# Performance work log

Measured on AMD Instinct MI355X. Metric: run time of the kernel, lower is better.

Reference implementation:

```python
import jax, jax.numpy as jnp
import numpy as np

WINDOW = 13

def setup_inputs() -> dict:
    key = jax.random.key(0)
    ks = jax.random.split(key, 5)
    B, C, D, H, W = 8, 64, 13, 64, 64
    c8 = C // 8
    x = jax.random.normal(ks[0], (B, C, D, H, W), dtype=jnp.float32)
    wq = jax.random.normal(ks[1], (c8, C), dtype=jnp.float32) * 0.1
    wk = jax.random.normal(ks[2], (c8, C), dtype=jnp.float32) * 0.1
    wv = jax.random.normal(ks[3], (C, C), dtype=jnp.float32) * 0.1
    bq = jnp.zeros((c8,), jnp.float32)
    bk = jnp.zeros((c8,), jnp.float32)
    bv = jnp.zeros((C,), jnp.float32)
    return {"x": x, "wq": wq, "bq": bq, "wk": wk, "bk": bk, "wv": wv, "bv": bv}

def reference(x, wq, bq, wk, bk, wv, bv):
    B, C, D, H, W = x.shape
    N = D * H * W
    nb = N // WINDOW  # N chosen divisible by WINDOW
    xf = x.reshape(B, C, N)
    # 1x1 Conv3d == per-voxel channel matmul
    q = jnp.einsum('oc,bcn->bon', wq, xf) + bq[None, :, None]
    k = jnp.einsum('oc,bcn->bon', wk, xf) + bk[None, :, None]
    v = jnp.einsum('oc,bcn->bon', wv, xf) + bv[None, :, None]
    # split flattened spatial dim into independent windows of size 13
    qb = q.reshape(B, -1, nb, WINDOW)
    kb = k.reshape(B, -1, nb, WINDOW)
    vb = v.reshape(B, C, nb, WINDOW)
    # scores[b,n,i,j] = sum_c q[b,c,n,i] * k[b,c,n,j]  (no scaling, as in source)
    scores = jnp.einsum('bcni,bcnj->bnij', qb, kb)
    att = jax.nn.softmax(scores, axis=-1)
    # out[b,c,n,i] = sum_j v[b,c,n,j] * att[b,n,i,j]  (v @ att^T per window)
    out = jnp.einsum('bcnj,bnij->bcni', vb, att)
    return out.reshape(B, C, D, H, W)
```

## Files before the change

### kernel.cpp

```cpp
#include <hip/hip_runtime.h>

#define WINDOW 13
#define NTOT   53248
#define WPB    8
#define VT     104
#define VS     112
#define WS     72
#define QKS    112
#define VPS    132

typedef float floatx4 __attribute__((ext_vector_type(4)));
typedef short shortx8 __attribute__((ext_vector_type(8)));

__device__ __forceinline__ unsigned short f2bf(float f) {
    union { float f; unsigned int u; } v; v.f = f;
    unsigned int u = v.u;
    unsigned int r = (u + 0x7fffu + ((u >> 16) & 1u)) >> 16;
    return (unsigned short)r;
}

__device__ __forceinline__ unsigned int pk2(float a, float b) {
    return (unsigned int)f2bf(a) | ((unsigned int)f2bf(b) << 16);
}

__global__ __launch_bounds__(512, 6)
void attn_win13_kernel(const float* __restrict__ x,
                       const float* __restrict__ wq, const float* __restrict__ bq,
                       const float* __restrict__ wk, const float* __restrict__ bk,
                       const float* __restrict__ wv, const float* __restrict__ bv,
                       float* __restrict__ out)
{
    __shared__ __align__(16) unsigned short xT[VS * WS];
    __shared__ __align__(16) unsigned short wbf[80 * WS];
    __shared__ float ball[80];
    __shared__ __align__(16) unsigned short vpad[64 * VPS];
    __shared__ __align__(16) float qk[16 * QKS];
    float* const att = (float*)wbf;
    unsigned short* const attb = (unsigned short*)qk;

    const int tid = threadIdx.x;
    const int b   = blockIdx.y;
    const int v0  = blockIdx.x * VT;
    const size_t total = (size_t)512 * NTOT;

    if (tid < 224) {
        const int vq = tid >> 3, cg8 = tid & 7;
        const int c0 = cg8 * 8, vx = vq * 4;
        float xv[4][8];
#pragma unroll
        for (int i = 0; i < 8; ++i) {
            size_t idx = (size_t)(b * 64 + c0 + i) * NTOT + v0 + vx;
            if (idx > total - 4) idx = total - 4;
            const float4 t = *(const float4*)(x + idx);
            xv[0][i] = t.x; xv[1][i] = t.y; xv[2][i] = t.z; xv[3][i] = t.w;
        }
#pragma unroll
        for (int r = 0; r < 4; ++r) {
            uint4 pk;
            pk.x = pk2(xv[r][0], xv[r][1]);
            pk.y = pk2(xv[r][2], xv[r][3]);
            pk.z = pk2(xv[r][4], xv[r][5]);
            pk.w = pk2(xv[r][6], xv[r][7]);
            *(uint4*)(&xT[(vx + r) * WS + c0]) = pk;
        }
    } else if (tid >= 256) {
        const int wf0 = tid - 256;
#pragma unroll
        for (int it = 0; it < 3; ++it) {
            const int wf = wf0 + (it << 8);
            if (wf < 640) {
                const int r = wf >> 3, cw = (wf & 7) * 8;
                const float* src = (r < 8)  ? (wq + r * 64 + cw)
                                 : (r < 16) ? (wk + (r - 8) * 64 + cw)
                                            : (wv + (r - 16) * 64 + cw);
                const float4 w0 = *(const float4*)src;
                const float4 w1 = *(const float4*)(src + 4);
                uint4 pk;
                pk.x = pk2(w0.x, w0.y); pk.y = pk2(w0.z, w0.w);
                pk.z = pk2(w1.x, w1.y); pk.w = pk2(w1.z, w1.w);
                *(uint4*)(&wbf[r * WS + cw]) = pk;
            }
        }
    }
    if (tid >= 432) {
        const int t2 = tid - 432;
        ball[t2] = (t2 < 8) ? bq[t2] : (t2 < 16) ? bk[t2 - 8] : bv[t2 - 16];
    }
    {
        const int r = tid >> 3, w = tid & 7;
        vpad[r * VPS + w * 16 + 13] = 0;
        *(unsigned int*)(&vpad[r * VPS + w * 16 + 14]) = 0u;
    }
    __syncthreads();

    {
        const int wid  = tid >> 6;
        const int lane = tid & 63;
        const int col  = lane & 15;
        const int g    = lane >> 4;
        for (int t = wid; t < 35; t += 8) {
            const int mt = t / 7, nt = t % 7;
            const shortx8 wa0 = *(const shortx8*)(&wbf[(mt * 16 + col) * WS + g * 8]);
            const shortx8 xa0 = *(const shortx8*)(&xT [(nt * 16 + col) * WS + g * 8]);
            const shortx8 wa1 = *(const shortx8*)(&wbf[(mt * 16 + col) * WS + 32 + g * 8]);
            const shortx8 xa1 = *(const shortx8*)(&xT [(nt * 16 + col) * WS + 32 + g * 8]);
            floatx4 acc = {0.f, 0.f, 0.f, 0.f};
            if (mt == 0) {
                acc = __builtin_amdgcn_mfma_f32_16x16x32_bf16(wa0, xa0, acc, 0, 0, 0);
                acc = __builtin_amdgcn_mfma_f32_16x16x32_bf16(wa1, xa1, acc, 0, 0, 0);
                const int row0 = g * 4;
                const int vox  = nt * 16 + col;
                qk[(row0 + 0) * QKS + vox] = acc[0] + ball[row0 + 0];
                qk[(row0 + 1) * QKS + vox] = acc[1] + ball[row0 + 1];
                qk[(row0 + 2) * QKS + vox] = acc[2] + ball[row0 + 2];
                qk[(row0 + 3) * QKS + vox] = acc[3] + ball[row0 + 3];
            } else {
                acc = __builtin_amdgcn_mfma_f32_16x16x32_bf16(xa0, wa0, acc, 0, 0, 0);
                acc = __builtin_amdgcn_mfma_f32_16x16x32_bf16(xa1, wa1, acc, 0, 0, 0);
                const int c_out = (mt - 1) * 16 + col;
                const float bias = ball[16 + c_out];
                int vox = nt * 16 + g * 4;
                int w = vox / 13, j = vox - w * 13;
#pragma unroll
                for (int r = 0; r < 4; ++r) {
                    if (vox + r < VT)
                        vpad[c_out * VPS + w * 16 + j] = f2bf(acc[r] + bias);
                    if (++j == 13) { j = 0; ++w; }
                }
            }
        }
    }
    __syncthreads();

    for (int f = tid; f < WPB * 169; f += 512) {
        const int w = f / 169, rem = f % 169;
        const int i = rem / 13, j = rem % 13;
        const float* qp = &qk[w * 13 + i];
        const float* kp = &qk[w * 13 + j];
        float s = 0.f;
#pragma unroll
        for (int o = 0; o < 8; ++o)
            s += qp[o * QKS] * kp[(8 + o) * QKS];
        att[f] = s;
    }
    __syncthreads();

    if (tid < WPB * WINDOW) {
        const int w = tid / 13, i = tid - w * 13;
        const float* row = att + w * 169 + i * 13;
        float m = row[0];
#pragma unroll
        for (int j = 1; j < 13; ++j) m = fmaxf(m, row[j]);
        float s0 = __expf(row[0] - m), s1 = __expf(row[1] - m), s2 = __expf(row[2] - m);
        float s3 = __expf(row[3] - m), s4 = __expf(row[4] - m), s5 = __expf(row[5] - m);
        float s6 = __expf(row[6] - m), s7 = __expf(row[7] - m), s8 = __expf(row[8] - m);
        float s9 = __expf(row[9] - m), sa = __expf(row[10] - m), sb = __expf(row[11] - m);
        float sc = __expf(row[12] - m);
        const float inv = 1.f / (s0+s1+s2+s3+s4+s5+s6+s7+s8+s9+sa+sb+sc);
        unsigned short* ab = attb + w * 256 + i * 16;
        uint4 lo, hi;
        lo.x = pk2(s0 * inv, s1 * inv); lo.y = pk2(s2 * inv, s3 * inv);
        lo.z = pk2(s4 * inv, s5 * inv); lo.w = pk2(s6 * inv, s7 * inv);
        hi.x = pk2(s8 * inv, s9 * inv); hi.y = pk2(sa * inv, sb * inv);
        hi.z = pk2(sc * inv, 0.f);      hi.w = 0u;
        *(uint4*)ab       = lo;
        *(uint4*)(ab + 8) = hi;
    }
    __syncthreads();

    {
        const int wid  = tid >> 6;
        const int lane = tid & 63;
        const int col  = lane & 15;
        const int g    = lane >> 4;
        const int gg   = (g & 1) * 8;
        shortx8 bfrag = *(const shortx8*)(&attb[wid * 256 + col * 16 + gg]);
        if (g & 2) bfrag = (shortx8){0, 0, 0, 0, 0, 0, 0, 0};
        const size_t obase = (size_t)(b * 64) * NTOT + v0 + wid * 13 + col;
#pragma unroll
        for (int ct = 0; ct < 4; ++ct) {
            const shortx8 afrag = *(const shortx8*)(&vpad[(ct * 16 + col) * VPS + wid * 16 + gg]);
            floatx4 acc = {0.f, 0.f, 0.f, 0.f};
            acc = __builtin_amdgcn_mfma_f32_16x16x32_bf16(afrag, bfrag, acc, 0, 0, 0);
            if (col < 13) {
                float* op = out + obase + (size_t)(ct * 16 + g * 4) * NTOT;
                op[0]                = acc[0];
                op[(size_t)NTOT]     = acc[1];
                op[(size_t)2 * NTOT] = acc[2];
                op[(size_t)3 * NTOT] = acc[3];
            }
        }
    }
}

extern "C" void kernel_launch(void* const* d_in, const int* in_sizes, int n_in,
                              void* d_out, int out_size, void* d_ws, size_t ws_size,
                              hipStream_t stream) {
    const float* x  = (const float*)d_in[0];
    const float* wq = (const float*)d_in[1];
    const float* bq = (const float*)d_in[2];
    const float* wk = (const float*)d_in[3];
    const float* bk = (const float*)d_in[4];
    const float* wv = (const float*)d_in[5];
    const float* bv = (const float*)d_in[6];
    float* out = (float*)d_out;

    dim3 grid(NTOT / VT, 8);
    dim3 block(512);
    attn_win13_kernel<<<grid, block, 0, stream>>>(x, wq, bq, wk, bk, wv, bv, out);
}
```

Measured before the change: 233.2 us.

## Switch to fp16 MFMA, halve tile, compute scores via MFMA with shuffle softmax

Several changes land together. Weight conversion moves into a separate prep kernel that writes fp16 weights and biases to the workspace, and all MFMAs switch from bf16 to fp16. The tile per block shrinks from 8 windows to 4, and the scalar QK^T score loop is replaced by an MFMA plus a wave-shuffle softmax, which removes one barrier and the fp32 score buffer. The intent is to cut per-block LDS and scalar work and raise occupancy, at the cost of an extra kernel launch, more blocks, and fp16 range risk.

```diff
diff --git a/kernel.cpp b/kernel.cpp
--- a/kernel.cpp
+++ b/kernel.cpp
@@ -2,94 +2,100 @@
 
 #define WINDOW 13
 #define NTOT   53248
-#define WPB    8
-#define VT     104
-#define VS     112
-#define WS     72
-#define QKS    112
-#define VPS    132
-
-typedef float floatx4 __attribute__((ext_vector_type(4)));
-typedef short shortx8 __attribute__((ext_vector_type(8)));
-
-__device__ __forceinline__ unsigned short f2bf(float f) {
-    union { float f; unsigned int u; } v; v.f = f;
-    unsigned int u = v.u;
-    unsigned int r = (u + 0x7fffu + ((u >> 16) & 1u)) >> 16;
-    return (unsigned short)r;
-}
-
-__device__ __forceinline__ unsigned int pk2(float a, float b) {
-    return (unsigned int)f2bf(a) | ((unsigned int)f2bf(b) << 16);
-}
-
-__global__ __launch_bounds__(512, 6)
+#define WPB    4
+#define VT     52
+#define VS     64
+#define XS     72
+#define QKTS   24
+
+typedef float  floatx4 __attribute__((ext_vector_type(4)));
+typedef _Float16 f16x8 __attribute__((ext_vector_type(8)));
+typedef __fp16   fp16x2 __attribute__((ext_vector_type(2)));
+
+__device__ __forceinline__ unsigned int pkh2(float a, float b) {
+    union { fp16x2 h; unsigned int u; } c;
+    c.h = __builtin_amdgcn_cvt_pkrtz(a, b);
+    return c.u;
+}
+__device__ __forceinline__ unsigned short cvt1(float a) {
+    union { _Float16 h; unsigned short u; } c;
+    c.h = (_Float16)a;
+    return c.u;
+}
+
+__global__ __launch_bounds__(256)
+void prep_kernel(const float* __restrict__ wq, const float* __restrict__ bq,
+                 const float* __restrict__ wk, const float* __restrict__ bk,
+                 const float* __restrict__ wv, const float* __restrict__ bv,
+                 unsigned short* __restrict__ ws)
+{
+    const int f = blockIdx.x * 256 + threadIdx.x;
+    if (f < 640) {
+        const int r = f >> 3, cw = (f & 7) * 8;
+        const float* src = (r < 8)  ? (wq + r * 64 + cw)
+                         : (r < 16) ? (wk + (r - 8) * 64 + cw)
+                                    : (wv + (r - 16) * 64 + cw);
+        const float4 w0 = *(const float4*)src;
+        const float4 w1 = *(const float4*)(src + 4);
+        uint4 pk;
+        pk.x = pkh2(w0.x, w0.y); pk.y = pkh2(w0.z, w0.w);
+        pk.z = pkh2(w1.x, w1.y); pk.w = pkh2(w1.z, w1.w);
+        *(uint4*)(ws + r * 64 + cw) = pk;
+    } else if (f < 720) {
+        const int t = f - 640;
+        const float bb = (t < 8) ? bq[t] : (t < 16) ? bk[t - 8] : bv[t - 16];
+        ((float*)(ws + 5120))[t] = bb;
+    }
+}
+
+__global__ __launch_bounds__(512, 8)
 void attn_win13_kernel(const float* __restrict__ x,
-                       const float* __restrict__ wq, const float* __restrict__ bq,
-                       const float* __restrict__ wk, const float* __restrict__ bk,
-                       const float* __restrict__ wv, const float* __restrict__ bv,
+                       const unsigned short* __restrict__ ws,
                        float* __restrict__ out)
 {
-    __shared__ __align__(16) unsigned short xT[VS * WS];
-    __shared__ __align__(16) unsigned short wbf[80 * WS];
+    __shared__ __align__(16) unsigned short xT[VS * XS];
+    __shared__ __align__(16) unsigned short wbf[80 * XS];
     __shared__ float ball[80];
-    __shared__ __align__(16) unsigned short vpad[64 * VPS];
-    __shared__ __align__(16) float qk[16 * QKS];
-    float* const att = (float*)wbf;
-    unsigned short* const attb = (unsigned short*)qk;
+    __shared__ __align__(16) unsigned short vpad[64 * XS];
+    __shared__ __align__(16) unsigned short qkT[VS * QKTS];
+    unsigned short* const attb = (unsigned short*)wbf;
 
     const int tid = threadIdx.x;
     const int b   = blockIdx.y;
     const int v0  = blockIdx.x * VT;
     const size_t total = (size_t)512 * NTOT;
 
-    if (tid < 224) {
-        const int vq = tid >> 3, cg8 = tid & 7;
-        const int c0 = cg8 * 8, vx = vq * 4;
-        float xv[4][8];
-#pragma unroll
-        for (int i = 0; i < 8; ++i) {
-            size_t idx = (size_t)(b * 64 + c0 + i) * NTOT + v0 + vx;
-            if (idx > total - 4) idx = total - 4;
-            const float4 t = *(const float4*)(x + idx);
-            xv[0][i] = t.x; xv[1][i] = t.y; xv[2][i] = t.z; xv[3][i] = t.w;
-        }
-#pragma unroll
-        for (int r = 0; r < 4; ++r) {
-            uint4 pk;
-            pk.x = pk2(xv[r][0], xv[r][1]);
-            pk.y = pk2(xv[r][2], xv[r][3]);
-            pk.z = pk2(xv[r][4], xv[r][5]);
-            pk.w = pk2(xv[r][6], xv[r][7]);
-            *(uint4*)(&xT[(vx + r) * WS + c0]) = pk;
-        }
-    } else if (tid >= 256) {
-        const int wf0 = tid - 256;
-#pragma unroll
-        for (int it = 0; it < 3; ++it) {
-            const int wf = wf0 + (it << 8);
-            if (wf < 640) {
-                const int r = wf >> 3, cw = (wf & 7) * 8;
-                const float* src = (r < 8)  ? (wq + r * 64 + cw)
-                                 : (r < 16) ? (wk + (r - 8) * 64 + cw)
-                                            : (wv + (r - 16) * 64 + cw);
-                const float4 w0 = *(const float4*)src;
-                const float4 w1 = *(const float4*)(src + 4);
-                uint4 pk;
-                pk.x = pk2(w0.x, w0.y); pk.y = pk2(w0.z, w0.w);
-                pk.z = pk2(w1.x, w1.y); pk.w = pk2(w1.z, w1.w);
-                *(uint4*)(&wbf[r * WS + cw]) = pk;
+    {
+        const int vq = tid >> 5, cp = tid & 31;
+        const int c = cp * 2, vx = vq * 4;
+        size_t i0 = (size_t)(b * 64 + c) * NTOT + v0 + vx;
+        size_t i1 = i0 + NTOT;
+        if (i0 > total - 4) i0 = total - 4;
+        if (i1 > total - 4) i1 = total - 4;
+        const float4 x0 = *(const float4*)(x + i0);
+        const float4 x1 = *(const float4*)(x + i1);
+        *(unsigned int*)(&xT[(vx + 0) * XS + c]) = pkh2(x0.x, x1.x);
+        *(unsigned int*)(&xT[(vx + 1) * XS + c]) = pkh2(x0.y, x1.y);
+        *(unsigned int*)(&xT[(vx + 2) * XS + c]) = pkh2(x0.z, x1.z);
+        *(unsigned int*)(&xT[(vx + 3) * XS + c]) = pkh2(x0.w, x1.w);
+    }
+    {
+        int f = tid;
+#pragma unroll
+        for (int it = 0; it < 2; ++it, f += 512) {
+            if (f < 640) {
+                const int r = f >> 3, cw = (f & 7) * 8;
+                const uint4 pk = *(const uint4*)(ws + r * 64 + cw);
+                *(uint4*)(&wbf[r * XS + cw]) = pk;
             }
         }
     }
-    if (tid >= 432) {
-        const int t2 = tid - 432;
-        ball[t2] = (t2 < 8) ? bq[t2] : (t2 < 16) ? bk[t2 - 8] : bv[t2 - 16];
-    }
-    {
-        const int r = tid >> 3, w = tid & 7;
-        vpad[r * VPS + w * 16 + 13] = 0;
-        *(unsigned int*)(&vpad[r * VPS + w * 16 + 14]) = 0u;
+    if (tid < 80) ball[tid] = ((const float*)(ws + 5120))[tid];
+    if (tid < 256) {
+        const int r = tid >> 2, w = tid & 3;
+        const int base = r * XS + w * 16;
+        vpad[base + 13] = 0;
+        *(unsigned int*)(&vpad[base + 14]) = 0u;
     }
     __syncthreads();
 
@@ -98,33 +104,28 @@
         const int lane = tid & 63;
         const int col  = lane & 15;
         const int g    = lane >> 4;
-        for (int t = wid; t < 35; t += 8) {
-            const int mt = t / 7, nt = t % 7;
-            const shortx8 wa0 = *(const shortx8*)(&wbf[(mt * 16 + col) * WS + g * 8]);
-            const shortx8 xa0 = *(const shortx8*)(&xT [(nt * 16 + col) * WS + g * 8]);
-            const shortx8 wa1 = *(const shortx8*)(&wbf[(mt * 16 + col) * WS + 32 + g * 8]);
-            const shortx8 xa1 = *(const shortx8*)(&xT [(nt * 16 + col) * WS + 32 + g * 8]);
+        for (int t = wid; t < 20; t += 8) {
+            const int mt = t >> 2, nt = t & 3;
+            const f16x8 xa0 = *(const f16x8*)(&xT [(nt * 16 + col) * XS + g * 8]);
+            const f16x8 wa0 = *(const f16x8*)(&wbf[(mt * 16 + col) * XS + g * 8]);
+            const f16x8 xa1 = *(const f16x8*)(&xT [(nt * 16 + col) * XS + 32 + g * 8]);
+            const f16x8 wa1 = *(const f16x8*)(&wbf[(mt * 16 + col) * XS + 32 + g * 8]);
             floatx4 acc = {0.f, 0.f, 0.f, 0.f};
+            acc = __builtin_amdgcn_mfma_f32_16x16x32_f16(xa0, wa0, acc, 0, 0, 0);
+            acc = __builtin_amdgcn_mfma_f32_16x16x32_f16(xa1, wa1, acc, 0, 0, 0);
+            const int vox = nt * 16 + g * 4;
             if (mt == 0) {
-                acc = __builtin_amdgcn_mfma_f32_16x16x32_bf16(wa0, xa0, acc, 0, 0, 0);
-                acc = __builtin_amdgcn_mfma_f32_16x16x32_bf16(wa1, xa1, acc, 0, 0, 0);
-                const int row0 = g * 4;
-                const int vox  = nt * 16 + col;
-                qk[(row0 + 0) * QKS + vox] = acc[0] + ball[row0 + 0];
-                qk[(row0 + 1) * QKS + vox] = acc[1] + ball[row0 + 1];
-                qk[(row0 + 2) * QKS + vox] = acc[2] + ball[row0 + 2];
-                qk[(row0 + 3) * QKS + vox] = acc[3] + ball[row0 + 3];
+                const float qkb = ball[col];
+#pragma unroll
+                for (int r = 0; r < 4; ++r)
+                    qkT[(vox + r) * QKTS + col] = cvt1(acc[r] + qkb);
             } else {
-                acc = __builtin_amdgcn_mfma_f32_16x16x32_bf16(xa0, wa0, acc, 0, 0, 0);
-                acc = __builtin_amdgcn_mfma_f32_16x16x32_bf16(xa1, wa1, acc, 0, 0, 0);
                 const int c_out = (mt - 1) * 16 + col;
-                const float bias = ball[16 + c_out];
-                int vox = nt * 16 + g * 4;
+                const float vb = ball[16 + c_out];
                 int w = vox / 13, j = vox - w * 13;
 #pragma unroll
                 for (int r = 0; r < 4; ++r) {
-                    if (vox + r < VT)
-                        vpad[c_out * VPS + w * 16 + j] = f2bf(acc[r] + bias);
+                    if (w < WPB) vpad[c_out * XS + w * 16 + j] = cvt1(acc[r] + vb);
                     if (++j == 13) { j = 0; ++w; }
                 }
             }
@@ -132,56 +133,51 @@
     }
     __syncthreads();
 
-    for (int f = tid; f < WPB * 169; f += 512) {
-        const int w = f / 169, rem = f % 169;
-        const int i = rem / 13, j = rem % 13;
-        const float* qp = &qk[w * 13 + i];
-        const float* kp = &qk[w * 13 + j];
-        float s = 0.f;
-#pragma unroll
-        for (int o = 0; o < 8; ++o)
-            s += qp[o * QKS] * kp[(8 + o) * QKS];
-        att[f] = s;
-    }
-    __syncthreads();
-
-    if (tid < WPB * WINDOW) {
-        const int w = tid / 13, i = tid - w * 13;
-        const float* row = att + w * 169 + i * 13;
-        float m = row[0];
-#pragma unroll
-        for (int j = 1; j < 13; ++j) m = fmaxf(m, row[j]);
-        float s0 = __expf(row[0] - m), s1 = __expf(row[1] - m), s2 = __expf(row[2] - m);
-        float s3 = __expf(row[3] - m), s4 = __expf(row[4] - m), s5 = __expf(row[5] - m);
-        float s6 = __expf(row[6] - m), s7 = __expf(row[7] - m), s8 = __expf(row[8] - m);
-        float s9 = __expf(row[9] - m), sa = __expf(row[10] - m), sb = __expf(row[11] - m);
-        float sc = __expf(row[12] - m);
-        const float inv = 1.f / (s0+s1+s2+s3+s4+s5+s6+s7+s8+s9+sa+sb+sc);
-        unsigned short* ab = attb + w * 256 + i * 16;
-        uint4 lo, hi;
-        lo.x = pk2(s0 * inv, s1 * inv); lo.y = pk2(s2 * inv, s3 * inv);
-        lo.z = pk2(s4 * inv, s5 * inv); lo.w = pk2(s6 * inv, s7 * inv);
-        hi.x = pk2(s8 * inv, s9 * inv); hi.y = pk2(sa * inv, sb * inv);
-        hi.z = pk2(sc * inv, 0.f);      hi.w = 0u;
-        *(uint4*)ab       = lo;
-        *(uint4*)(ab + 8) = hi;
-    }
-    __syncthreads();
-
-    {
+    if (tid < 256) {
         const int wid  = tid >> 6;
         const int lane = tid & 63;
         const int col  = lane & 15;
         const int g    = lane >> 4;
-        const int gg   = (g & 1) * 8;
-        shortx8 bfrag = *(const shortx8*)(&attb[wid * 256 + col * 16 + gg]);
-        if (g & 2) bfrag = (shortx8){0, 0, 0, 0, 0, 0, 0, 0};
-        const size_t obase = (size_t)(b * 64) * NTOT + v0 + wid * 13 + col;
-#pragma unroll
-        for (int ct = 0; ct < 4; ++ct) {
-            const shortx8 afrag = *(const shortx8*)(&vpad[(ct * 16 + col) * VPS + wid * 16 + gg]);
+        const f16x8 z = {};
+        const f16x8 af = (g < 2) ? *(const f16x8*)(&qkT[(wid * 13 + col) * QKTS + g * 8]) : z;
+        const f16x8 bf = (g == 0) ? *(const f16x8*)(&qkT[(wid * 13 + col) * QKTS + 8]) : z;
+        floatx4 acc = {0.f, 0.f, 0.f, 0.f};
+        acc = __builtin_amdgcn_mfma_f32_16x16x32_f16(af, bf, acc, 0, 0, 0);
+#pragma unroll
+        for (int r = 0; r < 4; ++r) {
+            const float s = (col < 13) ? acc[r] : -1e30f;
+            float m = s;
+            m = fmaxf(m, __shfl_xor(m, 1));
+            m = fmaxf(m, __shfl_xor(m, 2));
+            m = fmaxf(m, __shfl_xor(m, 4));
+            m = fmaxf(m, __shfl_xor(m, 8));
+            const float e = __expf(s - m);
+            float sum = e;
+            sum += __shfl_xor(sum, 1);
+            sum += __shfl_xor(sum, 2);
+            sum += __shfl_xor(sum, 4);
+            sum += __shfl_xor(sum, 8);
+            attb[wid * 256 + (g * 4 + r) * 16 + col] = cvt1(e / sum);
+        }
+    }
+    __syncthreads();
+
+    {
+        const int wid  = tid >> 6;
+        const int lane = tid & 63;
+        const int col  = lane & 15;
+        const int g    = lane >> 4;
+        const int gA   = g & 1;
+        const int w    = wid >> 1;
+        const f16x8 z = {};
+        const f16x8 bfrag = (g < 2) ? *(const f16x8*)(&attb[w * 256 + col * 16 + g * 8]) : z;
+        const size_t obase = (size_t)(b * 64) * NTOT + v0 + w * 13 + col;
+#pragma unroll
+        for (int q = 0; q < 2; ++q) {
+            const int ct = (wid & 1) * 2 + q;
+            const f16x8 afrag = *(const f16x8*)(&vpad[(ct * 16 + col) * XS + w * 16 + gA * 8]);
             floatx4 acc = {0.f, 0.f, 0.f, 0.f};
-            acc = __builtin_amdgcn_mfma_f32_16x16x32_bf16(afrag, bfrag, acc, 0, 0, 0);
+            acc = __builtin_amdgcn_mfma_f32_16x16x32_f16(afrag, bfrag, acc, 0, 0, 0);
             if (col < 13) {
                 float* op = out + obase + (size_t)(ct * 16 + g * 4) * NTOT;
                 op[0]                = acc[0];
@@ -204,8 +200,11 @@
     const float* wv = (const float*)d_in[5];
     const float* bv = (const float*)d_in[6];
     float* out = (float*)d_out;
+    unsigned short* ws = (unsigned short*)d_ws;
+
+    prep_kernel<<<dim3(3), dim3(256), 0, stream>>>(wq, bq, wk, bk, wv, bv, ws);
 
     dim3 grid(NTOT / VT, 8);
     dim3 block(512);
-    attn_win13_kernel<<<grid, block, 0, stream>>>(x, wq, bq, wk, bk, wv, bv, out);
-}
+    attn_win13_kernel<<<grid, block, 0, stream>>>(x, ws, out);
+}
```

Measured after the change: 246.4 us. 5.7% more time.
